# Kernel tuning notes

Measured on AMD Instinct MI355X. Metric: run time of the kernel, lower is better.

The kernel has to match this reference:

```python
import jax, jax.numpy as jnp
import numpy as np

B, T, I, H, O = 32, 128, 256, 256, 128

def setup_inputs() -> dict:
    key = jax.random.key(0)
    k = jax.random.split(key, 7)
    init_k = 1.0 / np.sqrt(H)
    sentence = jax.random.normal(k[0], (B, T, I), dtype=jnp.float32)
    weight_lambda = jax.random.uniform(k[1], (H, H + I), minval=0.0, maxval=1.0, dtype=jnp.float32)
    weight_gamma = jax.random.uniform(k[2], (H, H + I), minval=-0.001 * init_k, maxval=0.001 * init_k, dtype=jnp.float32)
    weight = jax.random.uniform(k[3], (H, H + I), minval=-init_k, maxval=init_k, dtype=jnp.float32)
    bias = jax.random.uniform(k[4], (H,), minval=-init_k, maxval=init_k, dtype=jnp.float32)
    W_out = jax.random.uniform(k[5], (O, H), minval=-init_k, maxval=init_k, dtype=jnp.float32)
    b_out = jax.random.uniform(k[6], (O,), minval=-init_k, maxval=init_k, dtype=jnp.float32)
    return {"sentence": sentence, "weight_lambda": weight_lambda, "weight_gamma": weight_gamma,
            "weight": weight, "bias": bias, "W_out": W_out, "b_out": b_out}

def reference(sentence, weight_lambda, weight_gamma, weight, bias, W_out, b_out):
    b = sentence.shape[0]
    h0 = jnp.zeros((b, H), dtype=sentence.dtype)
    F0 = jnp.zeros((b, H, H + I), dtype=sentence.dtype)

    def step(carry, x_t):
        h, F = carry
        total_input = jnp.concatenate([x_t, h], axis=1)           # (B, I+H)
        total_weights = weight + F                                 # (B, H, I+H)
        h_new = jnp.tanh(jnp.einsum('bf,bhf->bh', total_input, total_weights) + bias)
        norm = jnp.linalg.norm(total_weights, axis=2, keepdims=True) + 1e-16  # (B, H, 1)
        h_new = h_new / norm[..., 0]
        F_new = weight_lambda * (F / norm) + weight_gamma * jnp.einsum('bf,bh->bhf', total_input, h_new)
        return (h_new, F_new), None

    (h_T, F_T), _ = jax.lax.scan(step, (h0, F0), jnp.swapaxes(sentence, 0, 1))
    tag_space = h_T @ W_out.T + b_out
    return tag_space, h_T, F_T
```

## Files before the change

kernel.cpp:

```cpp
#include <hip/hip_runtime.h>

#define BB 32
#define TT 128
#define II 256
#define HH 256
#define OO 128
#define FWID 512


typedef unsigned long long u64;

__device__ __forceinline__ u64 slot_ld(const u64* p) {
    return __hip_atomic_load(p, __ATOMIC_RELAXED, __HIP_MEMORY_SCOPE_AGENT);
}

__device__ __forceinline__ void gather_to_lds(const u64* base, int lane, unsigned us,
                                              float* dst, int* flag, int fval) {
    const u64* p = base + 4 * lane;
    u64 a, b, c, d;
    for (;;) {
        a = slot_ld(p);
        b = slot_ld(p + 1);
        c = slot_ld(p + 2);
        d = slot_ld(p + 3);
        bool ok = ((unsigned)(a >> 32) >= us) & ((unsigned)(b >> 32) >= us) &
                  ((unsigned)(c >> 32) >= us) & ((unsigned)(d >> 32) >= us);
        if (__all(ok)) break;
    }
    float4 hv;
    hv.x = __uint_as_float((unsigned)a);
    hv.y = __uint_as_float((unsigned)b);
    hv.z = __uint_as_float((unsigned)c);
    hv.w = __uint_as_float((unsigned)d);
    *reinterpret_cast<float4*>(dst + 4 * lane) = hv;
    if (lane == 0)
        __hip_atomic_store(flag, fval, __ATOMIC_RELEASE, __HIP_MEMORY_SCOPE_WORKGROUP);
}

__global__ __launch_bounds__(512, 2)
void stpn_kernel(const float* __restrict__ x,
                 const float* __restrict__ wlam,
                 const float* __restrict__ wgam,
                 const float* __restrict__ w,
                 const float* __restrict__ bias,
                 const float* __restrict__ wout,
                 const float* __restrict__ bout,
                 float* __restrict__ out,
                 u64* __restrict__ slots)
{
    __shared__ __align__(16) float lh[2][HH];
    __shared__ int lflag[2];

    const int tid  = threadIdx.x;
    const int bk   = blockIdx.x;
    const int b    = bk & 31;
    const int sl   = bk >> 5;
    const int wv   = tid >> 6;
    const int lane = tid & 63;
    const int g    = tid >> 4;
    const int i    = tid & 15;
    const int r    = sl * 32 + (g & 31);

    if (tid < 2) lflag[tid] = 0;

    float4 W4[8], L4[8], G4[8], F4[8];
    {
        const float4* wr = reinterpret_cast<const float4*>(w    + (size_t)r * FWID);
        const float4* lr = reinterpret_cast<const float4*>(wlam + (size_t)r * FWID);
        const float4* gr = reinterpret_cast<const float4*>(wgam + (size_t)r * FWID);
#pragma unroll
        for (int k = 0; k < 8; ++k) {
            W4[k] = wr[k * 16 + i];
            L4[k] = lr[k * 16 + i];
            G4[k] = gr[k * 16 + i];
            F4[k] = make_float4(0.f, 0.f, 0.f, 0.f);
        }
    }
    const float bj = bias[r];
    float hl = 0.f;

    __syncthreads();

    for (int s = 0; s < TT; ++s) {
        const int par = s & 1;

        const float4* xb = reinterpret_cast<const float4*>(x + ((size_t)b * TT + s) * II);
        float4 T0 = xb[i], T1 = xb[16 + i], T2 = xb[32 + i], T3 = xb[48 + i];

        float4 tw[4];
        float4 dx4 = make_float4(0,0,0,0), nv4 = make_float4(0,0,0,0);
        {
            float4 t;
            t.x = W4[0].x + F4[0].x; t.y = W4[0].y + F4[0].y; t.z = W4[0].z + F4[0].z; t.w = W4[0].w + F4[0].w;
            dx4.x = fmaf(T0.x, t.x, dx4.x); dx4.y = fmaf(T0.y, t.y, dx4.y);
            dx4.z = fmaf(T0.z, t.z, dx4.z); dx4.w = fmaf(T0.w, t.w, dx4.w);
            nv4.x = fmaf(t.x, t.x, nv4.x); nv4.y = fmaf(t.y, t.y, nv4.y);
            nv4.z = fmaf(t.z, t.z, nv4.z); nv4.w = fmaf(t.w, t.w, nv4.w);
            t.x = W4[1].x + F4[1].x; t.y = W4[1].y + F4[1].y; t.z = W4[1].z + F4[1].z; t.w = W4[1].w + F4[1].w;
            dx4.x = fmaf(T1.x, t.x, dx4.x); dx4.y = fmaf(T1.y, t.y, dx4.y);
            dx4.z = fmaf(T1.z, t.z, dx4.z); dx4.w = fmaf(T1.w, t.w, dx4.w);
            nv4.x = fmaf(t.x, t.x, nv4.x); nv4.y = fmaf(t.y, t.y, nv4.y);
            nv4.z = fmaf(t.z, t.z, nv4.z); nv4.w = fmaf(t.w, t.w, nv4.w);
            t.x = W4[2].x + F4[2].x; t.y = W4[2].y + F4[2].y; t.z = W4[2].z + F4[2].z; t.w = W4[2].w + F4[2].w;
            dx4.x = fmaf(T2.x, t.x, dx4.x); dx4.y = fmaf(T2.y, t.y, dx4.y);
            dx4.z = fmaf(T2.z, t.z, dx4.z); dx4.w = fmaf(T2.w, t.w, dx4.w);
            nv4.x = fmaf(t.x, t.x, nv4.x); nv4.y = fmaf(t.y, t.y, nv4.y);
            nv4.z = fmaf(t.z, t.z, nv4.z); nv4.w = fmaf(t.w, t.w, nv4.w);
            t.x = W4[3].x + F4[3].x; t.y = W4[3].y + F4[3].y; t.z = W4[3].z + F4[3].z; t.w = W4[3].w + F4[3].w;
            dx4.x = fmaf(T3.x, t.x, dx4.x); dx4.y = fmaf(T3.y, t.y, dx4.y);
            dx4.z = fmaf(T3.z, t.z, dx4.z); dx4.w = fmaf(T3.w, t.w, dx4.w);
            nv4.x = fmaf(t.x, t.x, nv4.x); nv4.y = fmaf(t.y, t.y, nv4.y);
            nv4.z = fmaf(t.z, t.z, nv4.z); nv4.w = fmaf(t.w, t.w, nv4.w);
#pragma unroll
            for (int k = 0; k < 4; ++k) {
                tw[k].x = W4[k + 4].x + F4[k + 4].x; tw[k].y = W4[k + 4].y + F4[k + 4].y;
                tw[k].z = W4[k + 4].z + F4[k + 4].z; tw[k].w = W4[k + 4].w + F4[k + 4].w;
                nv4.x = fmaf(tw[k].x, tw[k].x, nv4.x); nv4.y = fmaf(tw[k].y, tw[k].y, nv4.y);
                nv4.z = fmaf(tw[k].z, tw[k].z, nv4.z); nv4.w = fmaf(tw[k].w, tw[k].w, nv4.w);
            }
        }
        float dxs = (dx4.x + dx4.y) + (dx4.z + dx4.w);
        float nrm = (nv4.x + nv4.y) + (nv4.z + nv4.w);
#pragma unroll
        for (int off = 1; off <= 8; off <<= 1) {
            dxs += __shfl_xor(dxs, off, 64);
            nrm += __shfl_xor(nrm, off, 64);
        }
        const float invn = 1.0f / (sqrtf(nrm) + 1e-16f);

#pragma unroll
        for (int k = 0; k < 8; ++k) {
            F4[k].x = L4[k].x * (F4[k].x * invn); F4[k].y = L4[k].y * (F4[k].y * invn);
            F4[k].z = L4[k].z * (F4[k].z * invn); F4[k].w = L4[k].w * (F4[k].w * invn);
        }
        T0.x *= G4[0].x; T0.y *= G4[0].y; T0.z *= G4[0].z; T0.w *= G4[0].w;
        T1.x *= G4[1].x; T1.y *= G4[1].y; T1.z *= G4[1].z; T1.w *= G4[1].w;
        T2.x *= G4[2].x; T2.y *= G4[2].y; T2.z *= G4[2].z; T2.w *= G4[2].w;
        T3.x *= G4[3].x; T3.y *= G4[3].y; T3.z *= G4[3].z; T3.w *= G4[3].w;

        if (wv == 0) {
            gather_to_lds(slots + ((size_t)par * BB + b) * HH, lane,
                          (unsigned)s, lh[par], &lflag[par], s + 1);
        }

        while (__hip_atomic_load(&lflag[par], __ATOMIC_ACQUIRE, __HIP_MEMORY_SCOPE_WORKGROUP) <= s) {}
        const float4* lh4 = reinterpret_cast<const float4*>(lh[par]);
        float4 H0 = lh4[i], H1 = lh4[16 + i], H2 = lh4[32 + i], H3 = lh4[48 + i];

        float4 a4;
        a4.x = H0.x * tw[0].x; a4.y = H0.y * tw[0].y; a4.z = H0.z * tw[0].z; a4.w = H0.w * tw[0].w;
        a4.x = fmaf(H1.x, tw[1].x, a4.x); a4.y = fmaf(H1.y, tw[1].y, a4.y);
        a4.z = fmaf(H1.z, tw[1].z, a4.z); a4.w = fmaf(H1.w, tw[1].w, a4.w);
        a4.x = fmaf(H2.x, tw[2].x, a4.x); a4.y = fmaf(H2.y, tw[2].y, a4.y);
        a4.z = fmaf(H2.z, tw[2].z, a4.z); a4.w = fmaf(H2.w, tw[2].w, a4.w);
        a4.x = fmaf(H3.x, tw[3].x, a4.x); a4.y = fmaf(H3.y, tw[3].y, a4.y);
        a4.z = fmaf(H3.z, tw[3].z, a4.z); a4.w = fmaf(H3.w, tw[3].w, a4.w);
        float dh = (a4.x + a4.y) + (a4.z + a4.w);
#pragma unroll
        for (int off = 1; off <= 8; off <<= 1) dh += __shfl_xor(dh, off, 64);

        const float e = __expf(2.0f * (dxs + dh + bj));
        const float h = (1.0f - 2.0f / (e + 1.0f)) * invn;
        hl = h;

        if (i == 0) {
            __hip_atomic_store(slots + ((size_t)(par ^ 1) * BB + b) * HH + r,
                               ((u64)(unsigned)(s + 1) << 32) | (unsigned)__float_as_uint(h),
                               __ATOMIC_RELAXED, __HIP_MEMORY_SCOPE_AGENT);
        }

        F4[0].x = fmaf(T0.x, h, F4[0].x); F4[0].y = fmaf(T0.y, h, F4[0].y);
        F4[0].z = fmaf(T0.z, h, F4[0].z); F4[0].w = fmaf(T0.w, h, F4[0].w);
        F4[1].x = fmaf(T1.x, h, F4[1].x); F4[1].y = fmaf(T1.y, h, F4[1].y);
        F4[1].z = fmaf(T1.z, h, F4[1].z); F4[1].w = fmaf(T1.w, h, F4[1].w);
        F4[2].x = fmaf(T2.x, h, F4[2].x); F4[2].y = fmaf(T2.y, h, F4[2].y);
        F4[2].z = fmaf(T2.z, h, F4[2].z); F4[2].w = fmaf(T2.w, h, F4[2].w);
        F4[3].x = fmaf(T3.x, h, F4[3].x); F4[3].y = fmaf(T3.y, h, F4[3].y);
        F4[3].z = fmaf(T3.z, h, F4[3].z); F4[3].w = fmaf(T3.w, h, F4[3].w);
        F4[4].x = fmaf(G4[4].x * H0.x, h, F4[4].x); F4[4].y = fmaf(G4[4].y * H0.y, h, F4[4].y);
        F4[4].z = fmaf(G4[4].z * H0.z, h, F4[4].z); F4[4].w = fmaf(G4[4].w * H0.w, h, F4[4].w);
        F4[5].x = fmaf(G4[5].x * H1.x, h, F4[5].x); F4[5].y = fmaf(G4[5].y * H1.y, h, F4[5].y);
        F4[5].z = fmaf(G4[5].z * H1.z, h, F4[5].z); F4[5].w = fmaf(G4[5].w * H1.w, h, F4[5].w);
        F4[6].x = fmaf(G4[6].x * H2.x, h, F4[6].x); F4[6].y = fmaf(G4[6].y * H2.y, h, F4[6].y);
        F4[6].z = fmaf(G4[6].z * H2.z, h, F4[6].z); F4[6].w = fmaf(G4[6].w * H2.w, h, F4[6].w);
        F4[7].x = fmaf(G4[7].x * H3.x, h, F4[7].x); F4[7].y = fmaf(G4[7].y * H3.y, h, F4[7].y);
        F4[7].z = fmaf(G4[7].z * H3.z, h, F4[7].z); F4[7].w = fmaf(G4[7].w * H3.w, h, F4[7].w);
    }

    {
        float4* fo = reinterpret_cast<float4*>(out + 12288 + ((size_t)b * HH + r) * FWID);
#pragma unroll
        for (int k = 0; k < 8; ++k) fo[k * 16 + i] = F4[k];
    }
    if (i == 0) out[4096 + (size_t)b * HH + r] = hl;

    if (sl == 0) {
        if (wv == 0) {
            gather_to_lds(slots + ((size_t)(TT & 1) * BB + b) * HH, lane,
                          (unsigned)TT, lh[0], &lflag[0], TT + 1);
        }
        while (__hip_atomic_load(&lflag[0], __ATOMIC_ACQUIRE, __HIP_MEMORY_SCOPE_WORKGROUP) <= TT) {}
        if (tid < OO) {
            const float* hv = lh[0];
            float acc = bout[tid];
            const float* wo = wout + (size_t)tid * HH;
#pragma unroll 4
            for (int jj = 0; jj < HH; ++jj) acc = fmaf(wo[jj], hv[jj], acc);
            out[(size_t)b * OO + tid] = acc;
        }
    }
}

extern "C" void kernel_launch(void* const* d_in, const int* in_sizes, int n_in,
                              void* d_out, int out_size, void* d_ws, size_t ws_size,
                              hipStream_t stream) {
    (void)in_sizes; (void)n_in; (void)out_size; (void)ws_size;
    const float* x    = (const float*)d_in[0];
    const float* wlam = (const float*)d_in[1];
    const float* wgam = (const float*)d_in[2];
    const float* w    = (const float*)d_in[3];
    const float* bias = (const float*)d_in[4];
    const float* wout = (const float*)d_in[5];
    const float* bout = (const float*)d_in[6];
    float* out = (float*)d_out;

    u64* slots = (u64*)d_ws;

    hipMemsetAsync(d_ws, 0, 2ull * BB * HH * 8ull, stream);

    void* args[] = {(void*)&x, (void*)&wlam, (void*)&wgam, (void*)&w, (void*)&bias,
                    (void*)&wout, (void*)&bout, (void*)&out, (void*)&slots};
    hipLaunchCooperativeKernel((void*)stpn_kernel, dim3(256), dim3(512), args, 0, stream);
}
```

Measured before the change: 260.9 us.

## Use packed FP32 math, DPP reductions, rsq/rcp intrinsics, and prefetch next x

Rewrites the per-step inner math to use v_pk_fma/mul/add on float pairs, halving VALU instruction count. Replaces shfl_xor reductions with DPP row-shift adds, uses hardware rsq and rcp instead of sqrt+divide, and prefetches the next timestep's input before the F update. Inline asm may constrain scheduling. rsq drops the 1e-16 epsilon, and the DPP row_shr chain leaves the full 16-lane sum only in the last lane of each row rather than in all lanes, which looks incorrect.

```diff
diff --git a/kernel.cpp b/kernel.cpp
--- a/kernel.cpp
+++ b/kernel.cpp
@@ -9,6 +9,38 @@
 
 
 typedef unsigned long long u64;
+typedef float f32x2 __attribute__((ext_vector_type(2)));
+
+__device__ __forceinline__ f32x2 mk2(float a, float b) { f32x2 r; r.x = a; r.y = b; return r; }
+
+__device__ __forceinline__ f32x2 pk_fma(f32x2 a, f32x2 b, f32x2 c) {
+    f32x2 d;
+    asm("v_pk_fma_f32 %0, %1, %2, %3" : "=v"(d) : "v"(a), "v"(b), "v"(c));
+    return d;
+}
+__device__ __forceinline__ f32x2 pk_mul(f32x2 a, f32x2 b) {
+    f32x2 d;
+    asm("v_pk_mul_f32 %0, %1, %2" : "=v"(d) : "v"(a), "v"(b));
+    return d;
+}
+__device__ __forceinline__ f32x2 pk_add(f32x2 a, f32x2 b) {
+    f32x2 d;
+    asm("v_pk_add_f32 %0, %1, %2" : "=v"(d) : "v"(a), "v"(b));
+    return d;
+}
+
+template<int CTRL>
+__device__ __forceinline__ float dpp_add(float x) {
+    int t = __builtin_amdgcn_update_dpp(0, __float_as_int(x), CTRL, 0xF, 0xF, true);
+    return x + __int_as_float(t);
+}
+__device__ __forceinline__ float row16_sum(float x) {
+    x = dpp_add<0x128>(x);
+    x = dpp_add<0x124>(x);
+    x = dpp_add<0x122>(x);
+    x = dpp_add<0x121>(x);
+    return x;
+}
 
 __device__ __forceinline__ u64 slot_ld(const u64* p) {
     return __hip_atomic_load(p, __ATOMIC_RELAXED, __HIP_MEMORY_SCOPE_AGENT);
@@ -63,80 +95,63 @@
 
     if (tid < 2) lflag[tid] = 0;
 
-    float4 W4[8], L4[8], G4[8], F4[8];
+    f32x2 W2[16], Lm2[16], G2[16], F2[16];
     {
         const float4* wr = reinterpret_cast<const float4*>(w    + (size_t)r * FWID);
         const float4* lr = reinterpret_cast<const float4*>(wlam + (size_t)r * FWID);
         const float4* gr = reinterpret_cast<const float4*>(wgam + (size_t)r * FWID);
 #pragma unroll
         for (int k = 0; k < 8; ++k) {
-            W4[k] = wr[k * 16 + i];
-            L4[k] = lr[k * 16 + i];
-            G4[k] = gr[k * 16 + i];
-            F4[k] = make_float4(0.f, 0.f, 0.f, 0.f);
+            float4 t;
+            t = wr[k * 16 + i]; W2[2*k]  = mk2(t.x, t.y); W2[2*k+1]  = mk2(t.z, t.w);
+            t = lr[k * 16 + i]; Lm2[2*k] = mk2(t.x, t.y); Lm2[2*k+1] = mk2(t.z, t.w);
+            t = gr[k * 16 + i]; G2[2*k]  = mk2(t.x, t.y); G2[2*k+1]  = mk2(t.z, t.w);
+            F2[2*k] = mk2(0.f, 0.f); F2[2*k+1] = mk2(0.f, 0.f);
         }
     }
     const float bj = bias[r];
     float hl = 0.f;
 
+    float4 px0, px1, px2, px3;
+    {
+        const float4* xb4 = reinterpret_cast<const float4*>(x + (size_t)b * TT * II);
+        px0 = xb4[i]; px1 = xb4[16 + i]; px2 = xb4[32 + i]; px3 = xb4[48 + i];
+    }
+
     __syncthreads();
 
     for (int s = 0; s < TT; ++s) {
         const int par = s & 1;
 
-        const float4* xb = reinterpret_cast<const float4*>(x + ((size_t)b * TT + s) * II);
-        float4 T0 = xb[i], T1 = xb[16 + i], T2 = xb[32 + i], T3 = xb[48 + i];
-
-        float4 tw[4];
-        float4 dx4 = make_float4(0,0,0,0), nv4 = make_float4(0,0,0,0);
-        {
-            float4 t;
-            t.x = W4[0].x + F4[0].x; t.y = W4[0].y + F4[0].y; t.z = W4[0].z + F4[0].z; t.w = W4[0].w + F4[0].w;
-            dx4.x = fmaf(T0.x, t.x, dx4.x); dx4.y = fmaf(T0.y, t.y, dx4.y);
-            dx4.z = fmaf(T0.z, t.z, dx4.z); dx4.w = fmaf(T0.w, t.w, dx4.w);
-            nv4.x = fmaf(t.x, t.x, nv4.x); nv4.y = fmaf(t.y, t.y, nv4.y);
-            nv4.z = fmaf(t.z, t.z, nv4.z); nv4.w = fmaf(t.w, t.w, nv4.w);
-            t.x = W4[1].x + F4[1].x; t.y = W4[1].y + F4[1].y; t.z = W4[1].z + F4[1].z; t.w = W4[1].w + F4[1].w;
-            dx4.x = fmaf(T1.x, t.x, dx4.x); dx4.y = fmaf(T1.y, t.y, dx4.y);
-            dx4.z = fmaf(T1.z, t.z, dx4.z); dx4.w = fmaf(T1.w, t.w, dx4.w);
-            nv4.x = fmaf(t.x, t.x, nv4.x); nv4.y = fmaf(t.y, t.y, nv4.y);
-            nv4.z = fmaf(t.z, t.z, nv4.z); nv4.w = fmaf(t.w, t.w, nv4.w);
-            t.x = W4[2].x + F4[2].x; t.y = W4[2].y + F4[2].y; t.z = W4[2].z + F4[2].z; t.w = W4[2].w + F4[2].w;
-            dx4.x = fmaf(T2.x, t.x, dx4.x); dx4.y = fmaf(T2.y, t.y, dx4.y);
-            dx4.z = fmaf(T2.z, t.z, dx4.z); dx4.w = fmaf(T2.w, t.w, dx4.w);
-            nv4.x = fmaf(t.x, t.x, nv4.x); nv4.y = fmaf(t.y, t.y, nv4.y);
-            nv4.z = fmaf(t.z, t.z, nv4.z); nv4.w = fmaf(t.w, t.w, nv4.w);
-            t.x = W4[3].x + F4[3].x; t.y = W4[3].y + F4[3].y; t.z = W4[3].z + F4[3].z; t.w = W4[3].w + F4[3].w;
-            dx4.x = fmaf(T3.x, t.x, dx4.x); dx4.y = fmaf(T3.y, t.y, dx4.y);
-            dx4.z = fmaf(T3.z, t.z, dx4.z); dx4.w = fmaf(T3.w, t.w, dx4.w);
-            nv4.x = fmaf(t.x, t.x, nv4.x); nv4.y = fmaf(t.y, t.y, nv4.y);
-            nv4.z = fmaf(t.z, t.z, nv4.z); nv4.w = fmaf(t.w, t.w, nv4.w);
-#pragma unroll
-            for (int k = 0; k < 4; ++k) {
-                tw[k].x = W4[k + 4].x + F4[k + 4].x; tw[k].y = W4[k + 4].y + F4[k + 4].y;
-                tw[k].z = W4[k + 4].z + F4[k + 4].z; tw[k].w = W4[k + 4].w + F4[k + 4].w;
-                nv4.x = fmaf(tw[k].x, tw[k].x, nv4.x); nv4.y = fmaf(tw[k].y, tw[k].y, nv4.y);
-                nv4.z = fmaf(tw[k].z, tw[k].z, nv4.z); nv4.w = fmaf(tw[k].w, tw[k].w, nv4.w);
-            }
-        }
-        float dxs = (dx4.x + dx4.y) + (dx4.z + dx4.w);
-        float nrm = (nv4.x + nv4.y) + (nv4.z + nv4.w);
-#pragma unroll
-        for (int off = 1; off <= 8; off <<= 1) {
-            dxs += __shfl_xor(dxs, off, 64);
-            nrm += __shfl_xor(nrm, off, 64);
-        }
-        const float invn = 1.0f / (sqrtf(nrm) + 1e-16f);
-
-#pragma unroll
-        for (int k = 0; k < 8; ++k) {
-            F4[k].x = L4[k].x * (F4[k].x * invn); F4[k].y = L4[k].y * (F4[k].y * invn);
-            F4[k].z = L4[k].z * (F4[k].z * invn); F4[k].w = L4[k].w * (F4[k].w * invn);
-        }
-        T0.x *= G4[0].x; T0.y *= G4[0].y; T0.z *= G4[0].z; T0.w *= G4[0].w;
-        T1.x *= G4[1].x; T1.y *= G4[1].y; T1.z *= G4[1].z; T1.w *= G4[1].w;
-        T2.x *= G4[2].x; T2.y *= G4[2].y; T2.z *= G4[2].z; T2.w *= G4[2].w;
-        T3.x *= G4[3].x; T3.y *= G4[3].y; T3.z *= G4[3].z; T3.w *= G4[3].w;
+        f32x2 X2[8];
+        X2[0] = mk2(px0.x, px0.y); X2[1] = mk2(px0.z, px0.w);
+        X2[2] = mk2(px1.x, px1.y); X2[3] = mk2(px1.z, px1.w);
+        X2[4] = mk2(px2.x, px2.y); X2[5] = mk2(px2.z, px2.w);
+        X2[6] = mk2(px3.x, px3.y); X2[7] = mk2(px3.z, px3.w);
+
+        f32x2 tw2[8];
+        f32x2 dx2 = mk2(0.f, 0.f), nv2 = mk2(0.f, 0.f);
+#pragma unroll
+        for (int j = 0; j < 8; ++j) {
+            f32x2 t = pk_add(W2[j], F2[j]);
+            dx2 = pk_fma(X2[j], t, dx2);
+            nv2 = pk_fma(t, t, nv2);
+        }
+#pragma unroll
+        for (int j = 0; j < 8; ++j) {
+            tw2[j] = pk_add(W2[8 + j], F2[8 + j]);
+            nv2 = pk_fma(tw2[j], tw2[j], nv2);
+        }
+        float dxs = dx2.x + dx2.y;
+        float nrm = nv2.x + nv2.y;
+        dxs = row16_sum(dxs);
+        nrm = row16_sum(nrm);
+        const float invn = __builtin_amdgcn_rsqf(nrm);
+        const f32x2 invn2 = mk2(invn, invn);
+        const float dxb = dxs + bj;
+
+#pragma unroll
+        for (int j = 0; j < 16; ++j) F2[j] = pk_mul(Lm2[j], pk_mul(F2[j], invn2));
 
         if (wv == 0) {
             gather_to_lds(slots + ((size_t)par * BB + b) * HH, lane,
@@ -145,22 +160,27 @@
 
         while (__hip_atomic_load(&lflag[par], __ATOMIC_ACQUIRE, __HIP_MEMORY_SCOPE_WORKGROUP) <= s) {}
         const float4* lh4 = reinterpret_cast<const float4*>(lh[par]);
-        float4 H0 = lh4[i], H1 = lh4[16 + i], H2 = lh4[32 + i], H3 = lh4[48 + i];
-
-        float4 a4;
-        a4.x = H0.x * tw[0].x; a4.y = H0.y * tw[0].y; a4.z = H0.z * tw[0].z; a4.w = H0.w * tw[0].w;
-        a4.x = fmaf(H1.x, tw[1].x, a4.x); a4.y = fmaf(H1.y, tw[1].y, a4.y);
-        a4.z = fmaf(H1.z, tw[1].z, a4.z); a4.w = fmaf(H1.w, tw[1].w, a4.w);
-        a4.x = fmaf(H2.x, tw[2].x, a4.x); a4.y = fmaf(H2.y, tw[2].y, a4.y);
-        a4.z = fmaf(H2.z, tw[2].z, a4.z); a4.w = fmaf(H2.w, tw[2].w, a4.w);
-        a4.x = fmaf(H3.x, tw[3].x, a4.x); a4.y = fmaf(H3.y, tw[3].y, a4.y);
-        a4.z = fmaf(H3.z, tw[3].z, a4.z); a4.w = fmaf(H3.w, tw[3].w, a4.w);
-        float dh = (a4.x + a4.y) + (a4.z + a4.w);
-#pragma unroll
-        for (int off = 1; off <= 8; off <<= 1) dh += __shfl_xor(dh, off, 64);
-
-        const float e = __expf(2.0f * (dxs + dh + bj));
-        const float h = (1.0f - 2.0f / (e + 1.0f)) * invn;
+        float4 ha = lh4[i], hb = lh4[16 + i], hc = lh4[32 + i], hd = lh4[48 + i];
+        f32x2 H2[8];
+        H2[0] = mk2(ha.x, ha.y); H2[1] = mk2(ha.z, ha.w);
+        H2[2] = mk2(hb.x, hb.y); H2[3] = mk2(hb.z, hb.w);
+        H2[4] = mk2(hc.x, hc.y); H2[5] = mk2(hc.z, hc.w);
+        H2[6] = mk2(hd.x, hd.y); H2[7] = mk2(hd.z, hd.w);
+
+        f32x2 a2 = pk_mul(H2[0], tw2[0]);
+        f32x2 b2 = pk_mul(H2[1], tw2[1]);
+        a2 = pk_fma(H2[2], tw2[2], a2);
+        b2 = pk_fma(H2[3], tw2[3], b2);
+        a2 = pk_fma(H2[4], tw2[4], a2);
+        b2 = pk_fma(H2[5], tw2[5], b2);
+        a2 = pk_fma(H2[6], tw2[6], a2);
+        b2 = pk_fma(H2[7], tw2[7], b2);
+        f32x2 c2 = pk_add(a2, b2);
+        float dh = c2.x + c2.y;
+        dh = row16_sum(dh);
+
+        const float e = __expf(2.0f * (dxb + dh));
+        const float h = (1.0f - 2.0f * __builtin_amdgcn_rcpf(e + 1.0f)) * invn;
         hl = h;
 
         if (i == 0) {
@@ -169,28 +189,28 @@
                                __ATOMIC_RELAXED, __HIP_MEMORY_SCOPE_AGENT);
         }
 
-        F4[0].x = fmaf(T0.x, h, F4[0].x); F4[0].y = fmaf(T0.y, h, F4[0].y);
-        F4[0].z = fmaf(T0.z, h, F4[0].z); F4[0].w = fmaf(T0.w, h, F4[0].w);
-        F4[1].x = fmaf(T1.x, h, F4[1].x); F4[1].y = fmaf(T1.y, h, F4[1].y);
-        F4[1].z = fmaf(T1.z, h, F4[1].z); F4[1].w = fmaf(T1.w, h, F4[1].w);
-        F4[2].x = fmaf(T2.x, h, F4[2].x); F4[2].y = fmaf(T2.y, h, F4[2].y);
-        F4[2].z = fmaf(T2.z, h, F4[2].z); F4[2].w = fmaf(T2.w, h, F4[2].w);
-        F4[3].x = fmaf(T3.x, h, F4[3].x); F4[3].y = fmaf(T3.y, h, F4[3].y);
-        F4[3].z = fmaf(T3.z, h, F4[3].z); F4[3].w = fmaf(T3.w, h, F4[3].w);
-        F4[4].x = fmaf(G4[4].x * H0.x, h, F4[4].x); F4[4].y = fmaf(G4[4].y * H0.y, h, F4[4].y);
-        F4[4].z = fmaf(G4[4].z * H0.z, h, F4[4].z); F4[4].w = fmaf(G4[4].w * H0.w, h, F4[4].w);
-        F4[5].x = fmaf(G4[5].x * H1.x, h, F4[5].x); F4[5].y = fmaf(G4[5].y * H1.y, h, F4[5].y);
-        F4[5].z = fmaf(G4[5].z * H1.z, h, F4[5].z); F4[5].w = fmaf(G4[5].w * H1.w, h, F4[5].w);
-        F4[6].x = fmaf(G4[6].x * H2.x, h, F4[6].x); F4[6].y = fmaf(G4[6].y * H2.y, h, F4[6].y);
-        F4[6].z = fmaf(G4[6].z * H2.z, h, F4[6].z); F4[6].w = fmaf(G4[6].w * H2.w, h, F4[6].w);
-        F4[7].x = fmaf(G4[7].x * H3.x, h, F4[7].x); F4[7].y = fmaf(G4[7].y * H3.y, h, F4[7].y);
-        F4[7].z = fmaf(G4[7].z * H3.z, h, F4[7].z); F4[7].w = fmaf(G4[7].w * H3.w, h, F4[7].w);
+        if (s + 1 < TT) {
+            const float4* xn = reinterpret_cast<const float4*>(x + ((size_t)b * TT + (s + 1)) * II);
+            px0 = xn[i]; px1 = xn[16 + i]; px2 = xn[32 + i]; px3 = xn[48 + i];
+        }
+
+        const f32x2 h2v = mk2(h, h);
+#pragma unroll
+        for (int j = 0; j < 8; ++j)
+            F2[j] = pk_fma(pk_mul(X2[j], G2[j]), h2v, F2[j]);
+#pragma unroll
+        for (int j = 0; j < 8; ++j)
+            F2[8 + j] = pk_fma(pk_mul(G2[8 + j], H2[j]), h2v, F2[8 + j]);
     }
 
     {
         float4* fo = reinterpret_cast<float4*>(out + 12288 + ((size_t)b * HH + r) * FWID);
 #pragma unroll
-        for (int k = 0; k < 8; ++k) fo[k * 16 + i] = F4[k];
+        for (int k = 0; k < 8; ++k) {
+            float4 v;
+            v.x = F2[2*k].x; v.y = F2[2*k].y; v.z = F2[2*k+1].x; v.w = F2[2*k+1].y;
+            fo[k * 16 + i] = v;
+        }
     }
     if (i == 0) out[4096 + (size_t)b * HH + r] = hl;
 
```

New measurement: 265.8 us. Within noise of the previous version (+1.9%).
